# Kernel tuning notes

Measured on AMD Instinct MI355X. Metric: run time of the kernel, lower is better.

Reference implementation:

```python
import jax, jax.numpy as jnp
import numpy as np

EPS = 1e-5

def binarize(x):
    # det Binarize: sign with zeros mapped to +1
    return jnp.where(x >= 0, 1.0, -1.0).astype(x.dtype)

def conv3x3(x, w, stride=1):
    return jax.lax.conv_general_dilated(
        x, w, window_strides=(stride, stride), padding=((1, 1), (1, 1)),
        dimension_numbers=('NCHW', 'OIHW', 'NCHW'))

def batchnorm_train(x, gamma, beta):
    # training-mode BN: biased batch stats over (N, H, W)
    mean = jnp.mean(x, axis=(0, 2, 3), keepdims=True)
    var = jnp.mean(jnp.square(x - mean), axis=(0, 2, 3), keepdims=True)
    xn = (x - mean) * jax.lax.rsqrt(var + EPS)
    return xn * gamma[None, :, None, None] + beta[None, :, None, None]

def setup_inputs() -> dict:
    key = jax.random.key(0)
    k1, k2, k3 = jax.random.split(key, 3)
    C = 256
    return {
        'x': jax.random.normal(k1, (64, C, 28, 28), dtype=jnp.float32),
        'w1': jax.random.normal(k2, (C, C, 3, 3), dtype=jnp.float32) * 0.05,
        'w2': jax.random.normal(k3, (C, C, 3, 3), dtype=jnp.float32) * 0.05,
        'gamma1': jnp.ones((C,), jnp.float32),
        'beta1': jnp.zeros((C,), jnp.float32),
        'gamma2': jnp.ones((C,), jnp.float32),
        'beta2': jnp.zeros((C,), jnp.float32),
    }

def reference(x, w1, w2, gamma1, beta1, gamma2, beta2):
    residual = x
    # conv1: binarized activations and weights, 3x3 pad=1 stride=1
    out = conv3x3(binarize(x), binarize(w1))
    out = batchnorm_train(out, gamma1, beta1)
    out = jnp.clip(out, -1.0, 1.0)  # Hardtanh
    # conv2
    out = conv3x3(binarize(out), binarize(w2))
    out = out + residual
    # do_bntan
    out = batchnorm_train(out, gamma2, beta2)
    out = jnp.clip(out, -1.0, 1.0)
    return out
```

## Files before the change

kernel.cpp:

```cpp
#include <hip/hip_runtime.h>
#include <stdint.h>

typedef int v4i __attribute__((ext_vector_type(4)));

constexpr int C     = 256;
constexpr int H     = 28, W = 28;
constexpr int HW    = H * W;
constexpr int NB    = 64;
constexpr int GP    = NB * HW;
constexpr int CNT   = GP;
constexpr int TOTAL = NB * C * HW;
constexpr int MT    = 64;
constexpr int NBLK  = GP / MT;
constexpr int LROWS = 128;
constexpr int GPB   = GP / 256;

__global__ void pack_all_kernel(const float* __restrict__ pw1, const float* __restrict__ pw2,
                                const float* __restrict__ x,
                                v4i* __restrict__ wbf1, v4i* __restrict__ wbf2,
                                v4i* __restrict__ xb, double* __restrict__ stats) {
    const int t = threadIdx.x;
    const int bid = blockIdx.x;
    if (bid < 288) {
        const int gid = bid * 256 + t;
        const bool second = (gid >= 36864);
        const float* w = second ? pw2 : pw1;
        v4i* dst       = second ? wbf2 : wbf1;
        const int idx = second ? gid - 36864 : gid;
        const int l  = idx & 63;
        const int g  = (idx >> 6) & 15;
        const int kb = (idx >> 10) & 3;
        const int tp = idx >> 12;
        const int co  = g * 16 + (l & 15);
        const int ci0 = kb * 64 + (l >> 4) * 16;
        int b0 = 0, b1 = 0, b2 = 0, b3 = 0;
#pragma unroll
        for (int e = 0; e < 16; ++e) {
            float v = w[((size_t)co * C + ci0 + e) * 9 + tp];
            int b = (v < 0.f) ? 0xFF : 0x01;
            int sh = (e & 3) * 8;
            if (e < 4) b0 |= b << sh; else if (e < 8) b1 |= b << sh;
            else if (e < 12) b2 |= b << sh; else b3 |= b << sh;
        }
        v4i o; o.x = b0; o.y = b1; o.z = b2; o.w = b3;
        dst[idx] = o;
    } else {
        const int local = bid - 288;
        const int ch = local / GPB;
        const int gp = (local % GPB) * 256 + t;
        if (ch == 0 && gp < 1024) stats[gp] = 0.0;
        const int n = gp / HW, p = gp % HW;
        const float* base = x + (size_t)n * C * HW + p + (size_t)(ch * 16) * HW;
        int b0 = 0, b1 = 0, b2 = 0, b3 = 0;
#pragma unroll
        for (int e = 0; e < 16; ++e) {
            float v = base[(size_t)e * HW];
            int b = (v < 0.f) ? 0xFF : 0x01;
            int sh = (e & 3) * 8;
            if (e < 4) b0 |= b << sh; else if (e < 8) b1 |= b << sh;
            else if (e < 12) b2 |= b << sh; else b3 |= b << sh;
        }
        v4i o; o.x = b0; o.y = b1; o.z = b2; o.w = b3;
        xb[(size_t)ch * GP + gp] = o;
    }
}

__global__ void bn_signpack_kernel(const short* __restrict__ y,
                                   const double* __restrict__ sum,
                                   const double* __restrict__ sumsq,
                                   const float* __restrict__ gamma,
                                   const float* __restrict__ beta,
                                   v4i* __restrict__ xb) {
    __shared__ float s_scale[C], s_shift[C];
    const int t = threadIdx.x;
    {
        double mean = sum[t] / (double)CNT;
        double var  = sumsq[t] / (double)CNT - mean * mean;
        double inv  = 1.0 / sqrt(var + 1e-5);
        s_scale[t] = (float)inv * gamma[t];
        s_shift[t] = beta[t] - (float)(mean * inv) * gamma[t];
    }
    __syncthreads();
    const int local = blockIdx.x;
    const int ch = local / GPB;
    const int gp = (local % GPB) * 256 + t;
    const int n = gp / HW, p = gp % HW;
    const short* base = y + (size_t)n * C * HW + p + (size_t)(ch * 16) * HW;
    int b0 = 0, b1 = 0, b2 = 0, b3 = 0;
#pragma unroll
    for (int e = 0; e < 16; ++e) {
        const int c = ch * 16 + e;
        float z = (float)base[(size_t)e * HW] * s_scale[c] + s_shift[c];
        int b = (z < 0.f) ? 0xFF : 0x01;
        int sh = (e & 3) * 8;
        if (e < 4) b0 |= b << sh; else if (e < 8) b1 |= b << sh;
        else if (e < 12) b2 |= b << sh; else b3 |= b << sh;
    }
    v4i o; o.x = b0; o.y = b1; o.z = b2; o.w = b3;
    xb[(size_t)ch * GP + gp] = o;
}


#define ACC_DECL v4i c00={0,0,0,0},c01={0,0,0,0},c02={0,0,0,0},c03={0,0,0,0}, \
                     c10={0,0,0,0},c11={0,0,0,0},c12={0,0,0,0},c13={0,0,0,0}, \
                     c20={0,0,0,0},c21={0,0,0,0},c22={0,0,0,0},c23={0,0,0,0}, \
                     c30={0,0,0,0},c31={0,0,0,0},c32={0,0,0,0},c33={0,0,0,0};

#define MFMA(a,b,c) c = __builtin_amdgcn_mfma_i32_16x16x64_i8(a, b, c, 0, 0, 0);

#define B_LOADQ(P, idx) { const v4i* bp = wbf + (idx); \
    P##0 = bp[0]; P##1 = bp[64]; P##2 = bp[128]; P##3 = bp[192]; }

#define A_READQ(P, cb) { \
    P##0 = xl[R0 + ((cb) ^ S0)]; P##1 = xl[R1 + ((cb) ^ S1)]; \
    P##2 = xl[R2 + ((cb) ^ S2)]; P##3 = xl[R3 + ((cb) ^ S3)]; }

#define MFMA_Q(A,B) \
    __builtin_amdgcn_s_setprio(1); \
    MFMA(A##0,B##0,c00) MFMA(A##1,B##0,c10) MFMA(A##2,B##0,c20) MFMA(A##3,B##0,c30) \
    MFMA(A##0,B##1,c01) MFMA(A##1,B##1,c11) MFMA(A##2,B##1,c21) MFMA(A##3,B##1,c31) \
    MFMA(A##0,B##2,c02) MFMA(A##1,B##2,c12) MFMA(A##2,B##2,c22) MFMA(A##3,B##2,c32) \
    MFMA(A##0,B##3,c03) MFMA(A##1,B##3,c13) MFMA(A##2,B##3,c23) MFMA(A##3,B##3,c33) \
    __builtin_amdgcn_s_setprio(0);

#define TAPVARS(TPX, RD0,RD1,RD2,RD3, SD0,SD1,SD2,SD3) { \
    const int dr = (TPX)/3 - 1, dc = (TPX)%3 - 1; \
    const int lrb = 32 + llo + dr * W + dc; \
    const int sm = lrb & 15; \
    const bool m0 = ((unsigned)(cm0+dc) < 28u) && ((unsigned)(rm0+dr) < 28u); \
    const bool m1 = ((unsigned)(cm1+dc) < 28u) && ((unsigned)(rm1+dr) < 28u); \
    const bool m2 = ((unsigned)(cm2+dc) < 28u) && ((unsigned)(rm2+dr) < 28u); \
    const bool m3 = ((unsigned)(cm3+dc) < 28u) && ((unsigned)(rm3+dr) < 28u); \
    RD0 = m0 ? lrb*16        : 2048; SD0 = m0 ? sm : 0; \
    RD1 = m1 ? lrb*16 + 256  : 2048; SD1 = m1 ? sm : 0; \
    RD2 = m2 ? lrb*16 + 512  : 2048; SD2 = m2 ? sm : 0; \
    RD3 = m3 ? lrb*16 + 768  : 2048; SD3 = m3 ? sm : 0; }

#define EPIV(mt,ntl) { \
    const int gpv = gp0 + (mt)*16 + lhi*4; \
    const int nn = gpv / HW; const int pp = gpv - nn*HW; \
    const size_t base = (size_t)nn*(C*HW) + (size_t)(wn*64+(ntl)*16+llo)*HW + pp; \
    const v4i cc = c##mt##ntl; \
    if constexpr (HAS_RES) { \
        const float4 r = *(const float4*)(residual + base); \
        float4 o; o.x = (float)cc.x + r.x; o.y = (float)cc.y + r.y; \
        o.z = (float)cc.z + r.z; o.w = (float)cc.w + r.w; \
        *(float4*)((float*)yout + base) = o; \
        sy##ntl += o.x + o.y + o.z + o.w; \
        sq##ntl += o.x*o.x + o.y*o.y + o.z*o.z + o.w*o.w; \
    } else { \
        int2 o; o.x = (cc.x & 0xFFFF) | (cc.y << 16); \
        o.y = (cc.z & 0xFFFF) | (cc.w << 16); \
        *(int2*)((short*)yout + base) = o; \
        const float fx = (float)cc.x, fy = (float)cc.y, fz = (float)cc.z, fw = (float)cc.w; \
        sy##ntl += fx + fy + fz + fw; \
        sq##ntl += fx*fx + fy*fy + fz*fz + fw*fw; \
    } }

#define REDN(ntl) { float s1 = sy##ntl, s2 = sq##ntl; \
    s1 += __shfl_down(s1, 32); s1 += __shfl_down(s1, 16); \
    s2 += __shfl_down(s2, 32); s2 += __shfl_down(s2, 16); \
    if (l < 16) { const int co = wn*64 + (ntl)*16 + l; \
        atomicAdd(&sum[co], (double)s1); atomicAdd(&sumsq[co], (double)s2); } }

template<bool HAS_RES, typename OUT_T>
__launch_bounds__(256, 3)
__global__ void bconv_mfma(const v4i* __restrict__ xb,
                           const v4i* __restrict__ wbf,
                           const float* __restrict__ residual,
                           OUT_T* __restrict__ yout,
                           double* __restrict__ sum, double* __restrict__ sumsq) {
    __shared__ v4i xl[LROWS * 16 + 16];
    const int t   = threadIdx.x;
    const int gp0 = blockIdx.x * MT;

#pragma unroll
    for (int pass = 0; pass < 8; ++pass) {
        const int i = pass * 256 + t;
        const int c = i >> 7;
        const int r = i & 127;
        int gsrc = min(max(gp0 - 32 + r, 0), GP - 1);
        xl[r * 16 + (c ^ (r & 15))] = xb[(size_t)c * GP + gsrc];
    }
    if (t < 16) { v4i z = {0,0,0,0}; xl[LROWS * 16 + t] = z; }
    __syncthreads();

    const int l = t & 63, wn = t >> 6;
    const int llo = l & 15, lhi = l >> 4;

    const int gx0 = gp0 + llo, gx1 = gx0 + 16, gx2 = gx0 + 32, gx3 = gx0 + 48;
    const int pm0 = gx0 % HW, pm1 = gx1 % HW, pm2 = gx2 % HW, pm3 = gx3 % HW;
    const int rm0 = pm0 / W, rm1 = pm1 / W, rm2 = pm2 / W, rm3 = pm3 / W;
    const int cm0 = pm0 % W, cm1 = pm1 % W, cm2 = pm2 % W, cm3 = pm3 % W;

    ACC_DECL
    const int bw = wn * 256 + l;

    int R0, R1, R2, R3, S0, S1, S2, S3;
    TAPVARS(0, R0,R1,R2,R3, S0,S1,S2,S3)
    v4i bP0,bP1,bP2,bP3, bQ0,bQ1,bQ2,bQ3;
    v4i aP0,aP1,aP2,aP3, aQ0,aQ1,aQ2,aQ3;
    B_LOADQ(bP, bw)
    A_READQ(aP, lhi)

#pragma unroll 1
    for (int tp = 0; tp < 9; ++tp) {
        const int tb = bw + tp * 4096;
        B_LOADQ(bQ, tb + 1024)
        A_READQ(aQ, 4 + lhi)
        MFMA_Q(aP, bP)
        B_LOADQ(bP, tb + 2048)
        A_READQ(aP, 8 + lhi)
        MFMA_Q(aQ, bQ)
        B_LOADQ(bQ, tb + 3072)
        A_READQ(aQ, 12 + lhi)
        MFMA_Q(aP, bP)
        const int tpn = (tp < 8) ? tp + 1 : 8;
        int N0, N1, N2, N3, T0, T1, T2, T3;
        TAPVARS(tpn, N0,N1,N2,N3, T0,T1,T2,T3)
        B_LOADQ(bP, bw + tpn * 4096)
        { aP0 = xl[N0 + (lhi ^ T0)]; aP1 = xl[N1 + (lhi ^ T1)];
          aP2 = xl[N2 + (lhi ^ T2)]; aP3 = xl[N3 + (lhi ^ T3)]; }
        MFMA_Q(aQ, bQ)
        R0 = N0; R1 = N1; R2 = N2; R3 = N3;
        S0 = T0; S1 = T1; S2 = T2; S3 = T3;
    }

    float sy0 = 0, sy1 = 0, sy2 = 0, sy3 = 0;
    float sq0 = 0, sq1 = 0, sq2 = 0, sq3 = 0;
    EPIV(0,0) EPIV(0,1) EPIV(0,2) EPIV(0,3)
    EPIV(1,0) EPIV(1,1) EPIV(1,2) EPIV(1,3)
    EPIV(2,0) EPIV(2,1) EPIV(2,2) EPIV(2,3)
    EPIV(3,0) EPIV(3,1) EPIV(3,2) EPIV(3,3)
    REDN(0) REDN(1) REDN(2) REDN(3)
}

__global__ void bn_clip_kernel(const float4* __restrict__ z,
                               const double* __restrict__ sum,
                               const double* __restrict__ sumsq,
                               const float* __restrict__ gamma,
                               const float* __restrict__ beta,
                               float4* __restrict__ out, int total4) {
    __shared__ float s_scale[C], s_shift[C];
    const int t = threadIdx.x;
    {
        double mean = sum[t] / (double)CNT;
        double var  = sumsq[t] / (double)CNT - mean * mean;
        double inv  = 1.0 / sqrt(var + 1e-5);
        s_scale[t] = (float)inv * gamma[t];
        s_shift[t] = beta[t] - (float)(mean * inv) * gamma[t];
    }
    __syncthreads();
    for (int i = blockIdx.x * blockDim.x + t; i < total4;
         i += gridDim.x * blockDim.x) {
        int c = (i / (HW / 4)) & (C - 1);
        float s = s_scale[c], b = s_shift[c];
        float4 v = z[i];
        v.x = fminf(1.f, fmaxf(-1.f, v.x * s + b));
        v.y = fminf(1.f, fmaxf(-1.f, v.y * s + b));
        v.z = fminf(1.f, fmaxf(-1.f, v.z * s + b));
        v.w = fminf(1.f, fmaxf(-1.f, v.w * s + b));
        out[i] = v;
    }
}

extern "C" void kernel_launch(void* const* d_in, const int* in_sizes, int n_in,
                              void* d_out, int out_size, void* d_ws, size_t ws_size,
                              hipStream_t stream) {
    const float* x  = (const float*)d_in[0];
    const float* w1 = (const float*)d_in[1];
    const float* w2 = (const float*)d_in[2];
    const float* g1 = (const float*)d_in[3];
    const float* b1 = (const float*)d_in[4];
    const float* g2 = (const float*)d_in[5];
    const float* b2 = (const float*)d_in[6];
    float* out = (float*)d_out;

    char* ws = (char*)d_ws;
    size_t off = 0;
    float* z2 = (float*)(ws + off);   off += (size_t)TOTAL * 4;
    v4i* xb1  = (v4i*)(ws + off);     off += (size_t)GP * 16 * 16;
    v4i* xb2  = (v4i*)(ws + off);     off += (size_t)GP * 16 * 16;
    v4i* wbf1 = (v4i*)(ws + off);     off += (size_t)36864 * 16;
    v4i* wbf2 = (v4i*)(ws + off);     off += (size_t)36864 * 16;
    double* stats = (double*)(ws + off); off += 4 * 256 * 8;
    double* sum1 = stats, *sumsq1 = stats + 256, *sum2 = stats + 512, *sumsq2 = stats + 768;

    short* y1 = (short*)d_out;

    pack_all_kernel<<<288 + 16 * GPB, 256, 0, stream>>>(w1, w2, x, wbf1, wbf2, xb1, stats);

    bconv_mfma<false, short><<<NBLK, 256, 0, stream>>>(xb1, wbf1, nullptr, y1, sum1, sumsq1);
    bn_signpack_kernel<<<16 * GPB, 256, 0, stream>>>(y1, sum1, sumsq1, g1, b1, xb2);
    bconv_mfma<true, float><<<NBLK, 256, 0, stream>>>(xb2, wbf2, x, z2, sum2, sumsq2);
    bn_clip_kernel<<<4096, 256, 0, stream>>>((const float4*)z2, sum2, sumsq2, g2, b2,
                                             (float4*)out, TOTAL / 4);
}
```

Measured before the change: 226.0 us.

## Fuse all stages into one cooperative persistent kernel with grid syncs

Replaces the five separate launches (pack, conv1, BN+signpack, conv2, BN+clip) with a single cooperative kernel of 768 blocks that runs each stage in turn, separated by grid-wide barriers. Leftover conv tiles are handled by 16 blocks doing a second tile. The aim is to remove kernel launch gaps and tail effects between stages. In exchange it adds grid.sync overhead and load imbalance from the extra tiles, and falls back to the old launch sequence if the cooperative launch fails.

```diff
diff --git a/kernel.cpp b/kernel.cpp
--- a/kernel.cpp
+++ b/kernel.cpp
@@ -1,6 +1,8 @@
 #include <hip/hip_runtime.h>
+#include <hip/hip_cooperative_groups.h>
 #include <stdint.h>
 
+namespace cg = cooperative_groups;
 typedef int v4i __attribute__((ext_vector_type(4)));
 
 constexpr int C     = 256;
@@ -14,74 +16,71 @@
 constexpr int NBLK  = GP / MT;
 constexpr int LROWS = 128;
 constexpr int GPB   = GP / 256;
-
-__global__ void pack_all_kernel(const float* __restrict__ pw1, const float* __restrict__ pw2,
-                                const float* __restrict__ x,
-                                v4i* __restrict__ wbf1, v4i* __restrict__ wbf2,
-                                v4i* __restrict__ xb, double* __restrict__ stats) {
-    const int t = threadIdx.x;
-    const int bid = blockIdx.x;
-    if (bid < 288) {
-        const int gid = bid * 256 + t;
-        const bool second = (gid >= 36864);
-        const float* w = second ? pw2 : pw1;
-        v4i* dst       = second ? wbf2 : wbf1;
-        const int idx = second ? gid - 36864 : gid;
-        const int l  = idx & 63;
-        const int g  = (idx >> 6) & 15;
-        const int kb = (idx >> 10) & 3;
-        const int tp = idx >> 12;
-        const int co  = g * 16 + (l & 15);
-        const int ci0 = kb * 64 + (l >> 4) * 16;
-        int b0 = 0, b1 = 0, b2 = 0, b3 = 0;
+constexpr int CGRID = 768;
+
+__device__ __forceinline__ void pack_w_item(int gid, const float* __restrict__ pw1,
+                                            const float* __restrict__ pw2,
+                                            v4i* __restrict__ wbf1, v4i* __restrict__ wbf2) {
+    const bool second = (gid >= 36864);
+    const float* w = second ? pw2 : pw1;
+    v4i* dst       = second ? wbf2 : wbf1;
+    const int idx = second ? gid - 36864 : gid;
+    const int l  = idx & 63;
+    const int g  = (idx >> 6) & 15;
+    const int kb = (idx >> 10) & 3;
+    const int tp = idx >> 12;
+    const int co  = g * 16 + (l & 15);
+    const int ci0 = kb * 64 + (l >> 4) * 16;
+    int b0 = 0, b1 = 0, b2 = 0, b3 = 0;
 #pragma unroll
-        for (int e = 0; e < 16; ++e) {
-            float v = w[((size_t)co * C + ci0 + e) * 9 + tp];
-            int b = (v < 0.f) ? 0xFF : 0x01;
-            int sh = (e & 3) * 8;
-            if (e < 4) b0 |= b << sh; else if (e < 8) b1 |= b << sh;
-            else if (e < 12) b2 |= b << sh; else b3 |= b << sh;
-        }
-        v4i o; o.x = b0; o.y = b1; o.z = b2; o.w = b3;
-        dst[idx] = o;
-    } else {
-        const int local = bid - 288;
-        const int ch = local / GPB;
-        const int gp = (local % GPB) * 256 + t;
-        if (ch == 0 && gp < 1024) stats[gp] = 0.0;
-        const int n = gp / HW, p = gp % HW;
-        const float* base = x + (size_t)n * C * HW + p + (size_t)(ch * 16) * HW;
-        int b0 = 0, b1 = 0, b2 = 0, b3 = 0;
+    for (int e = 0; e < 16; ++e) {
+        float v = w[((size_t)co * C + ci0 + e) * 9 + tp];
+        int b = (v < 0.f) ? 0xFF : 0x01;
+        int sh = (e & 3) * 8;
+        if (e < 4) b0 |= b << sh; else if (e < 8) b1 |= b << sh;
+        else if (e < 12) b2 |= b << sh; else b3 |= b << sh;
+    }
+    v4i o; o.x = b0; o.y = b1; o.z = b2; o.w = b3;
+    dst[idx] = o;
+}
+
+__device__ __forceinline__ void pack_x_item(int local, int t, const float* __restrict__ x,
+                                            v4i* __restrict__ xb, double* __restrict__ stats) {
+    const int ch = local / GPB;
+    const int gp = (local % GPB) * 256 + t;
+    if (ch == 0 && gp < 1024) stats[gp] = 0.0;
+    const int n = gp / HW, p = gp % HW;
+    const float* base = x + (size_t)n * C * HW + p + (size_t)(ch * 16) * HW;
+    int b0 = 0, b1 = 0, b2 = 0, b3 = 0;
 #pragma unroll
-        for (int e = 0; e < 16; ++e) {
-            float v = base[(size_t)e * HW];
-            int b = (v < 0.f) ? 0xFF : 0x01;
-            int sh = (e & 3) * 8;
-            if (e < 4) b0 |= b << sh; else if (e < 8) b1 |= b << sh;
-            else if (e < 12) b2 |= b << sh; else b3 |= b << sh;
-        }
-        v4i o; o.x = b0; o.y = b1; o.z = b2; o.w = b3;
-        xb[(size_t)ch * GP + gp] = o;
-    }
-}
-
-__global__ void bn_signpack_kernel(const short* __restrict__ y,
-                                   const double* __restrict__ sum,
-                                   const double* __restrict__ sumsq,
-                                   const float* __restrict__ gamma,
-                                   const float* __restrict__ beta,
-                                   v4i* __restrict__ xb) {
-    __shared__ float s_scale[C], s_shift[C];
-    const int t = threadIdx.x;
-    {
-        double mean = sum[t] / (double)CNT;
-        double var  = sumsq[t] / (double)CNT - mean * mean;
-        double inv  = 1.0 / sqrt(var + 1e-5);
-        s_scale[t] = (float)inv * gamma[t];
-        s_shift[t] = beta[t] - (float)(mean * inv) * gamma[t];
-    }
-    __syncthreads();
-    const int local = blockIdx.x;
+    for (int e = 0; e < 16; ++e) {
+        float v = base[(size_t)e * HW];
+        int b = (v < 0.f) ? 0xFF : 0x01;
+        int sh = (e & 3) * 8;
+        if (e < 4) b0 |= b << sh; else if (e < 8) b1 |= b << sh;
+        else if (e < 12) b2 |= b << sh; else b3 |= b << sh;
+    }
+    v4i o; o.x = b0; o.y = b1; o.z = b2; o.w = b3;
+    xb[(size_t)ch * GP + gp] = o;
+}
+
+__device__ __forceinline__ void finalize_coefs(int t, const double* __restrict__ sum,
+                                               const double* __restrict__ sumsq,
+                                               const float* __restrict__ gamma,
+                                               const float* __restrict__ beta,
+                                               float* __restrict__ s_scale,
+                                               float* __restrict__ s_shift) {
+    double mean = sum[t] / (double)CNT;
+    double var  = sumsq[t] / (double)CNT - mean * mean;
+    double inv  = 1.0 / sqrt(var + 1e-5);
+    s_scale[t] = (float)inv * gamma[t];
+    s_shift[t] = beta[t] - (float)(mean * inv) * gamma[t];
+}
+
+__device__ __forceinline__ void signpack_item(int local, int t, const short* __restrict__ y,
+                                              const float* __restrict__ s_scale,
+                                              const float* __restrict__ s_shift,
+                                              v4i* __restrict__ xb) {
     const int ch = local / GPB;
     const int gp = (local % GPB) * 256 + t;
     const int n = gp / HW, p = gp % HW;
@@ -98,6 +97,22 @@
     }
     v4i o; o.x = b0; o.y = b1; o.z = b2; o.w = b3;
     xb[(size_t)ch * GP + gp] = o;
+}
+
+__device__ __forceinline__ void clip_loop(int start, int stride, const float4* __restrict__ z4,
+                                          const float* __restrict__ s_scale,
+                                          const float* __restrict__ s_shift,
+                                          float4* __restrict__ out4) {
+    for (int i = start; i < TOTAL / 4; i += stride) {
+        int c = (i / (HW / 4)) & (C - 1);
+        float s = s_scale[c], b = s_shift[c];
+        float4 v = z4[i];
+        v.x = fminf(1.f, fmaxf(-1.f, v.x * s + b));
+        v.y = fminf(1.f, fmaxf(-1.f, v.y * s + b));
+        v.z = fminf(1.f, fmaxf(-1.f, v.z * s + b));
+        v.w = fminf(1.f, fmaxf(-1.f, v.w * s + b));
+        out4[i] = v;
+    }
 }
 
 
@@ -164,15 +179,16 @@
         atomicAdd(&sum[co], (double)s1); atomicAdd(&sumsq[co], (double)s2); } }
 
 template<bool HAS_RES, typename OUT_T>
-__launch_bounds__(256, 3)
-__global__ void bconv_mfma(const v4i* __restrict__ xb,
-                           const v4i* __restrict__ wbf,
-                           const float* __restrict__ residual,
-                           OUT_T* __restrict__ yout,
-                           double* __restrict__ sum, double* __restrict__ sumsq) {
-    __shared__ v4i xl[LROWS * 16 + 16];
-    const int t   = threadIdx.x;
-    const int gp0 = blockIdx.x * MT;
+__device__ __forceinline__ void conv_tile(const int tile, const int t,
+                                          v4i* __restrict__ xl,
+                                          const v4i* __restrict__ xb,
+                                          const v4i* __restrict__ wbf,
+                                          const float* __restrict__ residual,
+                                          OUT_T* __restrict__ yout,
+                                          double* __restrict__ sum,
+                                          double* __restrict__ sumsq) {
+    const int gp0 = tile * MT;
+    __syncthreads();
 
 #pragma unroll
     for (int pass = 0; pass < 8; ++pass) {
@@ -235,33 +251,96 @@
     REDN(0) REDN(1) REDN(2) REDN(3)
 }
 
+extern "C" __global__ void __launch_bounds__(256, 3)
+fused_all(const float* __restrict__ x,
+          const float* __restrict__ w1, const float* __restrict__ w2,
+          const float* __restrict__ g1, const float* __restrict__ b1,
+          const float* __restrict__ g2, const float* __restrict__ b2,
+          float* __restrict__ out, float* __restrict__ z2,
+          v4i* __restrict__ xb1, v4i* __restrict__ xb2,
+          v4i* __restrict__ wbf1, v4i* __restrict__ wbf2,
+          double* __restrict__ stats) {
+    cg::grid_group grid = cg::this_grid();
+    __shared__ v4i xl[LROWS * 16 + 16];
+    __shared__ float s_scale[C], s_shift[C];
+    const int t   = threadIdx.x;
+    const int bid = blockIdx.x;
+    const int nb  = gridDim.x;
+    double* sum1 = stats,       *sumsq1 = stats + 256;
+    double* sum2 = stats + 512, *sumsq2 = stats + 768;
+    short* y1 = (short*)out;
+
+    for (int vb = bid; vb < 288 + 16 * GPB; vb += nb) {
+        if (vb < 288) pack_w_item(vb * 256 + t, w1, w2, wbf1, wbf2);
+        else          pack_x_item(vb - 288, t, x, xb1, stats);
+    }
+    grid.sync();
+
+    conv_tile<false, short>(bid, t, xl, xb1, wbf1, nullptr, y1, sum1, sumsq1);
+    if ((bid % 48) == 0) conv_tile<false, short>(CGRID + bid / 48, t, xl, xb1, wbf1,
+                                                 nullptr, y1, sum1, sumsq1);
+    grid.sync();
+
+    finalize_coefs(t, sum1, sumsq1, g1, b1, s_scale, s_shift);
+    __syncthreads();
+    for (int vb = bid; vb < 16 * GPB; vb += nb)
+        signpack_item(vb, t, y1, s_scale, s_shift, xb2);
+    grid.sync();
+
+    conv_tile<true, float>(bid, t, xl, xb2, wbf2, x, z2, sum2, sumsq2);
+    if ((bid % 48) == 0) conv_tile<true, float>(CGRID + bid / 48, t, xl, xb2, wbf2,
+                                                x, z2, sum2, sumsq2);
+    grid.sync();
+
+    finalize_coefs(t, sum2, sumsq2, g2, b2, s_scale, s_shift);
+    __syncthreads();
+    clip_loop(bid * 256 + t, nb * 256, (const float4*)z2, s_scale, s_shift, (float4*)out);
+}
+
+__global__ void pack_all_kernel(const float* __restrict__ pw1, const float* __restrict__ pw2,
+                                const float* __restrict__ x,
+                                v4i* __restrict__ wbf1, v4i* __restrict__ wbf2,
+                                v4i* __restrict__ xb, double* __restrict__ stats) {
+    const int t = threadIdx.x, bid = blockIdx.x;
+    if (bid < 288) pack_w_item(bid * 256 + t, pw1, pw2, wbf1, wbf2);
+    else           pack_x_item(bid - 288, t, x, xb, stats);
+}
+
+__global__ void bn_signpack_kernel(const short* __restrict__ y,
+                                   const double* __restrict__ sum,
+                                   const double* __restrict__ sumsq,
+                                   const float* __restrict__ gamma,
+                                   const float* __restrict__ beta,
+                                   v4i* __restrict__ xb) {
+    __shared__ float s_scale[C], s_shift[C];
+    const int t = threadIdx.x;
+    finalize_coefs(t, sum, sumsq, gamma, beta, s_scale, s_shift);
+    __syncthreads();
+    signpack_item(blockIdx.x, t, y, s_scale, s_shift, xb);
+}
+
+template<bool HAS_RES, typename OUT_T>
+__launch_bounds__(256, 3)
+__global__ void bconv_mfma(const v4i* __restrict__ xb,
+                           const v4i* __restrict__ wbf,
+                           const float* __restrict__ residual,
+                           OUT_T* __restrict__ yout,
+                           double* __restrict__ sum, double* __restrict__ sumsq) {
+    __shared__ v4i xl[LROWS * 16 + 16];
+    conv_tile<HAS_RES, OUT_T>(blockIdx.x, threadIdx.x, xl, xb, wbf, residual, yout, sum, sumsq);
+}
+
 __global__ void bn_clip_kernel(const float4* __restrict__ z,
                                const double* __restrict__ sum,
                                const double* __restrict__ sumsq,
                                const float* __restrict__ gamma,
                                const float* __restrict__ beta,
-                               float4* __restrict__ out, int total4) {
+                               float4* __restrict__ out) {
     __shared__ float s_scale[C], s_shift[C];
     const int t = threadIdx.x;
-    {
-        double mean = sum[t] / (double)CNT;
-        double var  = sumsq[t] / (double)CNT - mean * mean;
-        double inv  = 1.0 / sqrt(var + 1e-5);
-        s_scale[t] = (float)inv * gamma[t];
-        s_shift[t] = beta[t] - (float)(mean * inv) * gamma[t];
-    }
-    __syncthreads();
-    for (int i = blockIdx.x * blockDim.x + t; i < total4;
-         i += gridDim.x * blockDim.x) {
-        int c = (i / (HW / 4)) & (C - 1);
-        float s = s_scale[c], b = s_shift[c];
-        float4 v = z[i];
-        v.x = fminf(1.f, fmaxf(-1.f, v.x * s + b));
-        v.y = fminf(1.f, fmaxf(-1.f, v.y * s + b));
-        v.z = fminf(1.f, fmaxf(-1.f, v.z * s + b));
-        v.w = fminf(1.f, fmaxf(-1.f, v.w * s + b));
-        out[i] = v;
-    }
+    finalize_coefs(t, sum, sumsq, gamma, beta, s_scale, s_shift);
+    __syncthreads();
+    clip_loop(blockIdx.x * 256 + t, gridDim.x * 256, z, s_scale, s_shift, out);
 }
 
 extern "C" void kernel_launch(void* const* d_in, const int* in_sizes, int n_in,
@@ -285,14 +364,20 @@
     v4i* wbf2 = (v4i*)(ws + off);     off += (size_t)36864 * 16;
     double* stats = (double*)(ws + off); off += 4 * 256 * 8;
     double* sum1 = stats, *sumsq1 = stats + 256, *sum2 = stats + 512, *sumsq2 = stats + 768;
-
     short* y1 = (short*)d_out;
 
-    pack_all_kernel<<<288 + 16 * GPB, 256, 0, stream>>>(w1, w2, x, wbf1, wbf2, xb1, stats);
-
-    bconv_mfma<false, short><<<NBLK, 256, 0, stream>>>(xb1, wbf1, nullptr, y1, sum1, sumsq1);
-    bn_signpack_kernel<<<16 * GPB, 256, 0, stream>>>(y1, sum1, sumsq1, g1, b1, xb2);
-    bconv_mfma<true, float><<<NBLK, 256, 0, stream>>>(xb2, wbf2, x, z2, sum2, sumsq2);
-    bn_clip_kernel<<<4096, 256, 0, stream>>>((const float4*)z2, sum2, sumsq2, g2, b2,
-                                             (float4*)out, TOTAL / 4);
-}
+    void* kargs[] = {(void*)&x, (void*)&w1, (void*)&w2, (void*)&g1, (void*)&b1,
+                     (void*)&g2, (void*)&b2, (void*)&out, (void*)&z2,
+                     (void*)&xb1, (void*)&xb2, (void*)&wbf1, (void*)&wbf2,
+                     (void*)&stats};
+    hipError_t err = hipLaunchCooperativeKernel(reinterpret_cast<void*>(fused_all),
+                                                dim3(CGRID), dim3(256), kargs, 0, stream);
+    if (err != hipSuccess) {
+        pack_all_kernel<<<288 + 16 * GPB, 256, 0, stream>>>(w1, w2, x, wbf1, wbf2, xb1, stats);
+        bconv_mfma<false, short><<<NBLK, 256, 0, stream>>>(xb1, wbf1, nullptr, y1, sum1, sumsq1);
+        bn_signpack_kernel<<<16 * GPB, 256, 0, stream>>>(y1, sum1, sumsq1, g1, b1, xb2);
+        bconv_mfma<true, float><<<NBLK, 256, 0, stream>>>(xb2, wbf2, x, z2, sum2, sumsq2);
+        bn_clip_kernel<<<4096, 256, 0, stream>>>((const float4*)z2, sum2, sumsq2, g2, b2,
+                                                 (float4*)out);
+    }
+}
```

Measured after the change: 630.2 us. 2.79x slower.

## Enlarge conv M-tile to 112 pixels and stage weight packing through LDS

Applied to the files above, without the earlier changes.

The binary conv kernel now covers 112 output pixels per block (7 M-subtiles instead of 4) with a 176-row LDS halo tile. Each weight fragment loaded from global memory therefore feeds more MFMAs, and the halo overhead per output shrinks. Launch bounds drop to 2 blocks per CU to make room for the larger accumulator set. Weight packing now reads each output-channel group with coalesced float4 loads into shared memory and transposes from there, replacing strided global gathers. The risks are register pressure and lower occupancy, and fewer blocks (448) for the GPU's CUs.

```diff
diff --git a/kernel.cpp b/kernel.cpp
--- a/kernel.cpp
+++ b/kernel.cpp
@@ -10,58 +10,85 @@
 constexpr int GP    = NB * HW;
 constexpr int CNT   = GP;
 constexpr int TOTAL = NB * C * HW;
-constexpr int MT    = 64;
+constexpr int MT    = 112;
 constexpr int NBLK  = GP / MT;
-constexpr int LROWS = 128;
+constexpr int LROWS = 176;
+constexpr int ZROW  = LROWS * 16;
 constexpr int GPB   = GP / 256;
+
+__device__ __forceinline__ void pack_x_item(int local, int t, const float* __restrict__ x,
+                                            v4i* __restrict__ xb, double* __restrict__ stats) {
+    const int ch = local / GPB;
+    const int gp = (local % GPB) * 256 + t;
+    if (ch == 0 && gp < 1024) stats[gp] = 0.0;
+    const int n = gp / HW, p = gp % HW;
+    const float* base = x + (size_t)n * C * HW + p + (size_t)(ch * 16) * HW;
+    int b0 = 0, b1 = 0, b2 = 0, b3 = 0;
+#pragma unroll
+    for (int e = 0; e < 16; ++e) {
+        float v = base[(size_t)e * HW];
+        int b = (v < 0.f) ? 0xFF : 0x01;
+        int sh = (e & 3) * 8;
+        if (e < 4) b0 |= b << sh; else if (e < 8) b1 |= b << sh;
+        else if (e < 12) b2 |= b << sh; else b3 |= b << sh;
+    }
+    v4i o; o.x = b0; o.y = b1; o.z = b2; o.w = b3;
+    xb[(size_t)ch * GP + gp] = o;
+}
+
+__device__ __forceinline__ void finalize_coefs(int t, const double* __restrict__ sum,
+                                               const double* __restrict__ sumsq,
+                                               const float* __restrict__ gamma,
+                                               const float* __restrict__ beta,
+                                               float* __restrict__ s_scale,
+                                               float* __restrict__ s_shift) {
+    double mean = sum[t] / (double)CNT;
+    double var  = sumsq[t] / (double)CNT - mean * mean;
+    double inv  = 1.0 / sqrt(var + 1e-5);
+    s_scale[t] = (float)inv * gamma[t];
+    s_shift[t] = beta[t] - (float)(mean * inv) * gamma[t];
+}
 
 __global__ void pack_all_kernel(const float* __restrict__ pw1, const float* __restrict__ pw2,
                                 const float* __restrict__ x,
                                 v4i* __restrict__ wbf1, v4i* __restrict__ wbf2,
                                 v4i* __restrict__ xb, double* __restrict__ stats) {
+    __shared__ signed char sgn[36864];
     const int t = threadIdx.x;
     const int bid = blockIdx.x;
-    if (bid < 288) {
-        const int gid = bid * 256 + t;
-        const bool second = (gid >= 36864);
-        const float* w = second ? pw2 : pw1;
-        v4i* dst       = second ? wbf2 : wbf1;
-        const int idx = second ? gid - 36864 : gid;
-        const int l  = idx & 63;
-        const int g  = (idx >> 6) & 15;
-        const int kb = (idx >> 10) & 3;
-        const int tp = idx >> 12;
-        const int co  = g * 16 + (l & 15);
-        const int ci0 = kb * 64 + (l >> 4) * 16;
-        int b0 = 0, b1 = 0, b2 = 0, b3 = 0;
+    if (bid < 32) {
+        const int g = bid & 15;
+        const float* w = (bid >> 4) ? pw2 : pw1;
+        v4i* dst       = (bid >> 4) ? wbf2 : wbf1;
+        const float4* wg = (const float4*)(w + (size_t)g * 16 * 2304);
+        int* sg4 = (int*)sgn;
+        for (int pass = 0; pass < 36; ++pass) {
+            const int m4 = pass * 256 + t;
+            float4 v = wg[m4];
+            int pk = (v.x < 0.f ? 0xFF : 0x01)
+                   | ((v.y < 0.f ? 0xFF : 0x01) << 8)
+                   | ((v.z < 0.f ? 0xFF : 0x01) << 16)
+                   | ((v.w < 0.f ? 0xFF : 0x01) << 24);
+            sg4[m4] = pk;
+        }
+        __syncthreads();
+        const int l = t & 63, kb = t >> 6;
+        const int colb = (l & 15) * 2304;
+        const int cib  = kb * 64 + (l >> 4) * 16;
+        for (int tp = 0; tp < 9; ++tp) {
+            int b0 = 0, b1 = 0, b2 = 0, b3 = 0;
 #pragma unroll
-        for (int e = 0; e < 16; ++e) {
-            float v = w[((size_t)co * C + ci0 + e) * 9 + tp];
-            int b = (v < 0.f) ? 0xFF : 0x01;
-            int sh = (e & 3) * 8;
-            if (e < 4) b0 |= b << sh; else if (e < 8) b1 |= b << sh;
-            else if (e < 12) b2 |= b << sh; else b3 |= b << sh;
+            for (int e = 0; e < 16; ++e) {
+                int b = (int)(unsigned char)sgn[colb + (cib + e) * 9 + tp];
+                int sh = (e & 3) * 8;
+                if (e < 4) b0 |= b << sh; else if (e < 8) b1 |= b << sh;
+                else if (e < 12) b2 |= b << sh; else b3 |= b << sh;
+            }
+            v4i o; o.x = b0; o.y = b1; o.z = b2; o.w = b3;
+            dst[((tp * 4 + kb) * 16 + g) * 64 + l] = o;
         }
-        v4i o; o.x = b0; o.y = b1; o.z = b2; o.w = b3;
-        dst[idx] = o;
     } else {
-        const int local = bid - 288;
-        const int ch = local / GPB;
-        const int gp = (local % GPB) * 256 + t;
-        if (ch == 0 && gp < 1024) stats[gp] = 0.0;
-        const int n = gp / HW, p = gp % HW;
-        const float* base = x + (size_t)n * C * HW + p + (size_t)(ch * 16) * HW;
-        int b0 = 0, b1 = 0, b2 = 0, b3 = 0;
-#pragma unroll
-        for (int e = 0; e < 16; ++e) {
-            float v = base[(size_t)e * HW];
-            int b = (v < 0.f) ? 0xFF : 0x01;
-            int sh = (e & 3) * 8;
-            if (e < 4) b0 |= b << sh; else if (e < 8) b1 |= b << sh;
-            else if (e < 12) b2 |= b << sh; else b3 |= b << sh;
-        }
-        v4i o; o.x = b0; o.y = b1; o.z = b2; o.w = b3;
-        xb[(size_t)ch * GP + gp] = o;
+        pack_x_item(bid - 32, t, x, xb, stats);
     }
 }
 
@@ -73,13 +100,7 @@
                                    v4i* __restrict__ xb) {
     __shared__ float s_scale[C], s_shift[C];
     const int t = threadIdx.x;
-    {
-        double mean = sum[t] / (double)CNT;
-        double var  = sumsq[t] / (double)CNT - mean * mean;
-        double inv  = 1.0 / sqrt(var + 1e-5);
-        s_scale[t] = (float)inv * gamma[t];
-        s_shift[t] = beta[t] - (float)(mean * inv) * gamma[t];
-    }
+    finalize_coefs(t, sum, sumsq, gamma, beta, s_scale, s_shift);
     __syncthreads();
     const int local = blockIdx.x;
     const int ch = local / GPB;
@@ -101,70 +122,67 @@
 }
 
 
-#define ACC_DECL v4i c00={0,0,0,0},c01={0,0,0,0},c02={0,0,0,0},c03={0,0,0,0}, \
-                     c10={0,0,0,0},c11={0,0,0,0},c12={0,0,0,0},c13={0,0,0,0}, \
-                     c20={0,0,0,0},c21={0,0,0,0},c22={0,0,0,0},c23={0,0,0,0}, \
-                     c30={0,0,0,0},c31={0,0,0,0},c32={0,0,0,0},c33={0,0,0,0};
+#define ACCD(m) v4i c##m##_0={0,0,0,0}, c##m##_1={0,0,0,0}, \
+                    c##m##_2={0,0,0,0}, c##m##_3={0,0,0,0};
+#define ACC_DECL ACCD(0) ACCD(1) ACCD(2) ACCD(3) ACCD(4) ACCD(5) ACCD(6)
 
 #define MFMA(a,b,c) c = __builtin_amdgcn_mfma_i32_16x16x64_i8(a, b, c, 0, 0, 0);
 
 #define B_LOADQ(P, idx) { const v4i* bp = wbf + (idx); \
     P##0 = bp[0]; P##1 = bp[64]; P##2 = bp[128]; P##3 = bp[192]; }
 
-#define A_READQ(P, cb) { \
-    P##0 = xl[R0 + ((cb) ^ S0)]; P##1 = xl[R1 + ((cb) ^ S1)]; \
-    P##2 = xl[R2 + ((cb) ^ S2)]; P##3 = xl[R3 + ((cb) ^ S3)]; }
-
-#define MFMA_Q(A,B) \
-    __builtin_amdgcn_s_setprio(1); \
-    MFMA(A##0,B##0,c00) MFMA(A##1,B##0,c10) MFMA(A##2,B##0,c20) MFMA(A##3,B##0,c30) \
-    MFMA(A##0,B##1,c01) MFMA(A##1,B##1,c11) MFMA(A##2,B##1,c21) MFMA(A##3,B##1,c31) \
-    MFMA(A##0,B##2,c02) MFMA(A##1,B##2,c12) MFMA(A##2,B##2,c22) MFMA(A##3,B##2,c32) \
-    MFMA(A##0,B##3,c03) MFMA(A##1,B##3,c13) MFMA(A##2,B##3,c23) MFMA(A##3,B##3,c33) \
+#define ARD(P, m, cb) P##m = xl[R##m + ((cb) ^ S##m)];
+#define ARDALL(P, cb) ARD(P,0,cb) ARD(P,1,cb) ARD(P,2,cb) ARD(P,3,cb) \
+                      ARD(P,4,cb) ARD(P,5,cb) ARD(P,6,cb)
+
+#define MFMAG(A,B,g) MFMA(A##0,B##g,c0_##g) MFMA(A##1,B##g,c1_##g) MFMA(A##2,B##g,c2_##g) \
+                     MFMA(A##3,B##g,c3_##g) MFMA(A##4,B##g,c4_##g) MFMA(A##5,B##g,c5_##g) \
+                     MFMA(A##6,B##g,c6_##g)
+#define MFMA_C(A,B) __builtin_amdgcn_s_setprio(1); \
+    MFMAG(A,B,0) MFMAG(A,B,1) MFMAG(A,B,2) MFMAG(A,B,3) \
     __builtin_amdgcn_s_setprio(0);
 
-#define TAPVARS(TPX, RD0,RD1,RD2,RD3, SD0,SD1,SD2,SD3) { \
-    const int dr = (TPX)/3 - 1, dc = (TPX)%3 - 1; \
-    const int lrb = 32 + llo + dr * W + dc; \
-    const int sm = lrb & 15; \
-    const bool m0 = ((unsigned)(cm0+dc) < 28u) && ((unsigned)(rm0+dr) < 28u); \
-    const bool m1 = ((unsigned)(cm1+dc) < 28u) && ((unsigned)(rm1+dr) < 28u); \
-    const bool m2 = ((unsigned)(cm2+dc) < 28u) && ((unsigned)(rm2+dr) < 28u); \
-    const bool m3 = ((unsigned)(cm3+dc) < 28u) && ((unsigned)(rm3+dr) < 28u); \
-    RD0 = m0 ? lrb*16        : 2048; SD0 = m0 ? sm : 0; \
-    RD1 = m1 ? lrb*16 + 256  : 2048; SD1 = m1 ? sm : 0; \
-    RD2 = m2 ? lrb*16 + 512  : 2048; SD2 = m2 ? sm : 0; \
-    RD3 = m3 ? lrb*16 + 768  : 2048; SD3 = m3 ? sm : 0; }
-
-#define EPIV(mt,ntl) { \
-    const int gpv = gp0 + (mt)*16 + lhi*4; \
+#define TV1(m) { const bool mk = ((unsigned)(cm##m + dc) < 28u) && \
+                                 ((unsigned)(rm##m + dr) < 28u); \
+    R##m = mk ? (lrb + 16 * (m)) * 16 : ZROW; S##m = mk ? sm : 0; }
+#define TAPVARS(TPX) { const int dr = (TPX)/3 - 1, dc = (TPX)%3 - 1; \
+    const int lrb = 32 + llo + dr * W + dc; const int sm = lrb & 15; \
+    TV1(0) TV1(1) TV1(2) TV1(3) TV1(4) TV1(5) TV1(6) }
+
+#define PMV(m) const int gx##m = gp0 + (m)*16 + llo; \
+    const int pmv##m = gx##m % HW; \
+    const int rm##m = pmv##m / W, cm##m = pmv##m % W;
+
+#define EPIV(m,g) { \
+    const int gpv = gp0 + (m)*16 + lhi*4; \
     const int nn = gpv / HW; const int pp = gpv - nn*HW; \
-    const size_t base = (size_t)nn*(C*HW) + (size_t)(wn*64+(ntl)*16+llo)*HW + pp; \
-    const v4i cc = c##mt##ntl; \
+    const size_t base = (size_t)nn*(C*HW) + (size_t)(wn*64+(g)*16+llo)*HW + pp; \
+    const v4i cc = c##m##_##g; \
     if constexpr (HAS_RES) { \
         const float4 r = *(const float4*)(residual + base); \
         float4 o; o.x = (float)cc.x + r.x; o.y = (float)cc.y + r.y; \
         o.z = (float)cc.z + r.z; o.w = (float)cc.w + r.w; \
         *(float4*)((float*)yout + base) = o; \
-        sy##ntl += o.x + o.y + o.z + o.w; \
-        sq##ntl += o.x*o.x + o.y*o.y + o.z*o.z + o.w*o.w; \
+        sy##g += o.x + o.y + o.z + o.w; \
+        sq##g += o.x*o.x + o.y*o.y + o.z*o.z + o.w*o.w; \
     } else { \
         int2 o; o.x = (cc.x & 0xFFFF) | (cc.y << 16); \
         o.y = (cc.z & 0xFFFF) | (cc.w << 16); \
         *(int2*)((short*)yout + base) = o; \
         const float fx = (float)cc.x, fy = (float)cc.y, fz = (float)cc.z, fw = (float)cc.w; \
-        sy##ntl += fx + fy + fz + fw; \
-        sq##ntl += fx*fx + fy*fy + fz*fz + fw*fw; \
+        sy##g += fx + fy + fz + fw; \
+        sq##g += fx*fx + fy*fy + fz*fz + fw*fw; \
     } }
-
-#define REDN(ntl) { float s1 = sy##ntl, s2 = sq##ntl; \
+#define EPIM(m) EPIV(m,0) EPIV(m,1) EPIV(m,2) EPIV(m,3)
+
+#define REDN(g) { float s1 = sy##g, s2 = sq##g; \
     s1 += __shfl_down(s1, 32); s1 += __shfl_down(s1, 16); \
     s2 += __shfl_down(s2, 32); s2 += __shfl_down(s2, 16); \
-    if (l < 16) { const int co = wn*64 + (ntl)*16 + l; \
+    if (l < 16) { const int co = wn*64 + (g)*16 + l; \
         atomicAdd(&sum[co], (double)s1); atomicAdd(&sumsq[co], (double)s2); } }
 
 template<bool HAS_RES, typename OUT_T>
-__launch_bounds__(256, 3)
+__launch_bounds__(256, 2)
 __global__ void bconv_mfma(const v4i* __restrict__ xb,
                            const v4i* __restrict__ wbf,
                            const float* __restrict__ residual,
@@ -174,64 +192,53 @@
     const int t   = threadIdx.x;
     const int gp0 = blockIdx.x * MT;
 
-#pragma unroll
-    for (int pass = 0; pass < 8; ++pass) {
+    for (int pass = 0; pass < 11; ++pass) {
         const int i = pass * 256 + t;
-        const int c = i >> 7;
-        const int r = i & 127;
+        const int c = i / LROWS;
+        const int r = i - c * LROWS;
         int gsrc = min(max(gp0 - 32 + r, 0), GP - 1);
         xl[r * 16 + (c ^ (r & 15))] = xb[(size_t)c * GP + gsrc];
     }
-    if (t < 16) { v4i z = {0,0,0,0}; xl[LROWS * 16 + t] = z; }
+    if (t < 16) { v4i z = {0,0,0,0}; xl[ZROW + t] = z; }
     __syncthreads();
 
     const int l = t & 63, wn = t >> 6;
     const int llo = l & 15, lhi = l >> 4;
 
-    const int gx0 = gp0 + llo, gx1 = gx0 + 16, gx2 = gx0 + 32, gx3 = gx0 + 48;
-    const int pm0 = gx0 % HW, pm1 = gx1 % HW, pm2 = gx2 % HW, pm3 = gx3 % HW;
-    const int rm0 = pm0 / W, rm1 = pm1 / W, rm2 = pm2 / W, rm3 = pm3 / W;
-    const int cm0 = pm0 % W, cm1 = pm1 % W, cm2 = pm2 % W, cm3 = pm3 % W;
+    PMV(0) PMV(1) PMV(2) PMV(3) PMV(4) PMV(5) PMV(6)
 
     ACC_DECL
     const int bw = wn * 256 + l;
 
-    int R0, R1, R2, R3, S0, S1, S2, S3;
-    TAPVARS(0, R0,R1,R2,R3, S0,S1,S2,S3)
+    int R0,R1,R2,R3,R4,R5,R6, S0,S1,S2,S3,S4,S5,S6;
+    TAPVARS(0)
     v4i bP0,bP1,bP2,bP3, bQ0,bQ1,bQ2,bQ3;
-    v4i aP0,aP1,aP2,aP3, aQ0,aQ1,aQ2,aQ3;
+    v4i aP0,aP1,aP2,aP3,aP4,aP5,aP6, aQ0,aQ1,aQ2,aQ3,aQ4,aQ5,aQ6;
     B_LOADQ(bP, bw)
-    A_READQ(aP, lhi)
+    ARDALL(aP, lhi)
 
 #pragma unroll 1
     for (int tp = 0; tp < 9; ++tp) {
         const int tb = bw + tp * 4096;
         B_LOADQ(bQ, tb + 1024)
-        A_READQ(aQ, 4 + lhi)
-        MFMA_Q(aP, bP)
+        ARDALL(aQ, 4 + lhi)
+        MFMA_C(aP, bP)
         B_LOADQ(bP, tb + 2048)
-        A_READQ(aP, 8 + lhi)
-        MFMA_Q(aQ, bQ)
+        ARDALL(aP, 8 + lhi)
+        MFMA_C(aQ, bQ)
         B_LOADQ(bQ, tb + 3072)
-        A_READQ(aQ, 12 + lhi)
-        MFMA_Q(aP, bP)
+        ARDALL(aQ, 12 + lhi)
+        MFMA_C(aP, bP)
         const int tpn = (tp < 8) ? tp + 1 : 8;
-        int N0, N1, N2, N3, T0, T1, T2, T3;
-        TAPVARS(tpn, N0,N1,N2,N3, T0,T1,T2,T3)
+        TAPVARS(tpn)
         B_LOADQ(bP, bw + tpn * 4096)
-        { aP0 = xl[N0 + (lhi ^ T0)]; aP1 = xl[N1 + (lhi ^ T1)];
-          aP2 = xl[N2 + (lhi ^ T2)]; aP3 = xl[N3 + (lhi ^ T3)]; }
-        MFMA_Q(aQ, bQ)
-        R0 = N0; R1 = N1; R2 = N2; R3 = N3;
-        S0 = T0; S1 = T1; S2 = T2; S3 = T3;
+        ARDALL(aP, lhi)
+        MFMA_C(aQ, bQ)
     }
 
     float sy0 = 0, sy1 = 0, sy2 = 0, sy3 = 0;
     float sq0 = 0, sq1 = 0, sq2 = 0, sq3 = 0;
-    EPIV(0,0) EPIV(0,1) EPIV(0,2) EPIV(0,3)
-    EPIV(1,0) EPIV(1,1) EPIV(1,2) EPIV(1,3)
-    EPIV(2,0) EPIV(2,1) EPIV(2,2) EPIV(2,3)
-    EPIV(3,0) EPIV(3,1) EPIV(3,2) EPIV(3,3)
+    EPIM(0) EPIM(1) EPIM(2) EPIM(3) EPIM(4) EPIM(5) EPIM(6)
     REDN(0) REDN(1) REDN(2) REDN(3)
 }
 
@@ -240,18 +247,12 @@
                                const double* __restrict__ sumsq,
                                const float* __restrict__ gamma,
                                const float* __restrict__ beta,
-                               float4* __restrict__ out, int total4) {
+                               float4* __restrict__ out) {
     __shared__ float s_scale[C], s_shift[C];
     const int t = threadIdx.x;
-    {
-        double mean = sum[t] / (double)CNT;
-        double var  = sumsq[t] / (double)CNT - mean * mean;
-        double inv  = 1.0 / sqrt(var + 1e-5);
-        s_scale[t] = (float)inv * gamma[t];
-        s_shift[t] = beta[t] - (float)(mean * inv) * gamma[t];
-    }
+    finalize_coefs(t, sum, sumsq, gamma, beta, s_scale, s_shift);
     __syncthreads();
-    for (int i = blockIdx.x * blockDim.x + t; i < total4;
+    for (int i = blockIdx.x * blockDim.x + t; i < TOTAL / 4;
          i += gridDim.x * blockDim.x) {
         int c = (i / (HW / 4)) & (C - 1);
         float s = s_scale[c], b = s_shift[c];
@@ -288,11 +289,11 @@
 
     short* y1 = (short*)d_out;
 
-    pack_all_kernel<<<288 + 16 * GPB, 256, 0, stream>>>(w1, w2, x, wbf1, wbf2, xb1, stats);
+    pack_all_kernel<<<32 + 16 * GPB, 256, 0, stream>>>(w1, w2, x, wbf1, wbf2, xb1, stats);
 
     bconv_mfma<false, short><<<NBLK, 256, 0, stream>>>(xb1, wbf1, nullptr, y1, sum1, sumsq1);
     bn_signpack_kernel<<<16 * GPB, 256, 0, stream>>>(y1, sum1, sumsq1, g1, b1, xb2);
     bconv_mfma<true, float><<<NBLK, 256, 0, stream>>>(xb2, wbf2, x, z2, sum2, sumsq2);
     bn_clip_kernel<<<4096, 256, 0, stream>>>((const float4*)z2, sum2, sumsq2, g2, b2,
-                                             (float4*)out, TOTAL / 4);
-}
+                                             (float4*)out);
+}
```

New measurement: 203.1 us. 1.11x faster.
